# Kernel optimization log

Hardware: AMD Instinct MI355X
Metric: run time of the kernel (lower is better)

The kernel has to match this reference:

```python
import jax, jax.numpy as jnp
import numpy as np

RADIUS = 0.4
NSAMPLE = 32
B, N, NPOINT, C = 4, 16384, 4096, 64


def _ball_query(xyz, new_xyz, radius, nsample):
    """PointNet++ ball query: first `nsample` point indices (in original order)
    within `radius` of each query; pad with the first found index (0 if none).
    xyz: (B,N,3)  new_xyz: (B,M,3)  ->  idx: (B,M,nsample) int32."""
    n = xyz.shape[1]
    # squared distances (B, M, N) via ||a||^2 + ||b||^2 - 2 a.b
    qq = jnp.sum(new_xyz * new_xyz, axis=-1)[:, :, None]
    pp = jnp.sum(xyz * xyz, axis=-1)[:, None, :]
    d2 = qq + pp - 2.0 * jnp.einsum('bmd,bnd->bmn', new_xyz, xyz)
    ar = jnp.arange(n, dtype=jnp.int32)
    # key = point index if inside ball else sentinel n; smallest keys = earliest hits
    key = jnp.where(d2 < radius * radius, ar, n)
    neg_small, _ = jax.lax.top_k(-key, nsample)   # nsample smallest keys
    sel = -neg_small                               # (B, M, nsample)
    valid = sel < n
    first = jnp.where(valid[..., :1], sel[..., :1], 0)
    return jnp.where(valid, sel, first).astype(jnp.int32)


def setup_inputs() -> dict:
    key = jax.random.key(0)
    k1, k2, k3 = jax.random.split(key, 3)
    xyz = jax.random.normal(k1, (B, N, 3), dtype=jnp.float32)
    new_xyz = jax.random.normal(k2, (B, NPOINT, 3), dtype=jnp.float32)
    features = jax.random.normal(k3, (B, C, N), dtype=jnp.float32)
    return {"xyz": xyz, "new_xyz": new_xyz, "features": features}


def reference(xyz, new_xyz, features):
    idx = _ball_query(xyz, new_xyz, RADIUS, NSAMPLE)            # (B, M, S)
    # gather xyz -> (B, M, S, 3) -> (B, 3, M, S), center on queries
    grouped_xyz = jax.vmap(lambda p, i: p[i])(xyz, idx)
    grouped_xyz = jnp.transpose(grouped_xyz, (0, 3, 1, 2))
    grouped_xyz = grouped_xyz - jnp.transpose(new_xyz, (0, 2, 1))[..., None]
    # gather features -> (B, C, M, S)
    grouped_feat = jax.vmap(lambda f, i: f[:, i])(features, idx)
    # use_xyz=True: concat centered coords with features on channel dim
    return jnp.concatenate([grouped_xyz, grouped_feat], axis=1)  # (B, 3+C, M, S)
```

## Files before the change

### kernel.cpp

```cpp
#include <hip/hip_runtime.h>
#include <stdint.h>

#define B_ 4
#define N_ 16384
#define M_ 4096
#define C_ 64
#define S_ 32
#define R2_ 0.16f
#define GDIM 32
#define CELLS 32768
#define CSTRIDE 32772

static const size_t OFF_XYZ4  = 0;
static const size_t OFF_FT    = (size_t)B_ * N_ * 4 * sizeof(float);
static const size_t OFF_IDX   = OFF_FT + (size_t)B_ * N_ * C_ * sizeof(float);
static const size_t OFF_START = OFF_FT;
static const size_t OFF_CUR   = OFF_START + (size_t)B_ * CSTRIDE * sizeof(int);
static const size_t OFF_SPTS  = OFF_CUR + (size_t)B_ * CSTRIDE * sizeof(int);
static const size_t OFF_SSID  = OFF_SPTS + (size_t)B_ * N_ * 4 * sizeof(float);

__device__ __forceinline__ int cellof(float v) {
    int c = (int)floorf((v + 8.0f) * 2.0f);
    return c < 0 ? 0 : (c > GDIM - 1 ? GDIM - 1 : c);
}

__global__ __launch_bounds__(256) void pack_hist(const float* __restrict__ xyz,
                                                 float4* __restrict__ xyz4,
                                                 int* __restrict__ cur) {
    int i = blockIdx.x * 256 + threadIdx.x;
    int b = i >> 14;
    float x = xyz[3 * i + 0];
    float y = xyz[3 * i + 1];
    float z = xyz[3 * i + 2];
    float pp = __fadd_rn(__fadd_rn(__fmul_rn(x, x), __fmul_rn(y, y)), __fmul_rn(z, z));
    xyz4[i] = make_float4(x, y, z, pp);
    int cid = (cellof(z) << 10) | (cellof(y) << 5) | cellof(x);
    atomicAdd(&cur[b * CSTRIDE + cid], 1);
}

__global__ __launch_bounds__(1024) void scan_cells(int* __restrict__ cur,
                                                   int* __restrict__ start) {
    __shared__ int ls[16];
    int b = blockIdx.x, t = threadIdx.x;
    int lane = t & 63, w = t >> 6;
    int* cb = cur + b * CSTRIDE;
    int* sb = start + b * CSTRIDE;
    int base = t * 32;
    int loc[32]; int tot = 0;
    #pragma unroll
    for (int j = 0; j < 32; ++j) { loc[j] = cb[base + j]; tot += loc[j]; }
    int pre = tot;
    #pragma unroll
    for (int o = 1; o < 64; o <<= 1) { int u = __shfl_up(pre, o); if (lane >= o) pre += u; }
    if (lane == 63) ls[w] = pre;
    __syncthreads();
    if (t < 16) {
        int v = ls[t];
        int p16 = v;
        #pragma unroll
        for (int o = 1; o < 16; o <<= 1) { int u = __shfl_up(p16, o); if (t >= o) p16 += u; }
        ls[t] = p16 - v;
    }
    __syncthreads();
    int run = ls[w] + (pre - tot);
    #pragma unroll
    for (int j = 0; j < 32; ++j) { sb[base + j] = run; cb[base + j] = run; run += loc[j]; }
    if (t == 0) sb[CELLS] = N_;
}

__global__ __launch_bounds__(256) void scatter_pts(const float4* __restrict__ xyz4,
                                                   int* __restrict__ cur,
                                                   float4* __restrict__ spts,
                                                   int* __restrict__ ssid) {
    int i = blockIdx.x * 256 + threadIdx.x;
    int b = i >> 14, n = i & (N_ - 1);
    float4 P = xyz4[i];
    int cid = (cellof(P.z) << 10) | (cellof(P.y) << 5) | cellof(P.x);
    int pos = atomicAdd(&cur[b * CSTRIDE + cid], 1);
    spts[(size_t)b * N_ + pos] = P;
    ssid[b * N_ + pos] = n;
}

__global__ __launch_bounds__(256) void ball_query_grid(const float4* __restrict__ spts,
                                                       const int* __restrict__ ssid,
                                                       const int* __restrict__ start,
                                                       const float* __restrict__ newxyz,
                                                       int* __restrict__ idx) {
    __shared__ unsigned int bmAll[4][512];
    __shared__ int bcAll[4];
    int tid = threadIdx.x, lane = tid & 63, w = tid >> 6;
    unsigned int* bm = bmAll[w];
    int gw = blockIdx.x * 4 + w;
    int b = gw >> 12;
    int m = gw & (M_ - 1);

    *(uint4*)&bm[lane * 8]     = make_uint4(0u, 0u, 0u, 0u);
    *(uint4*)&bm[lane * 8 + 4] = make_uint4(0u, 0u, 0u, 0u);
    if (lane == 0) bcAll[w] = 0;

    size_t qb = ((size_t)b * M_ + m) * 3;
    float qx = newxyz[qb + 0], qy = newxyz[qb + 1], qz = newxyz[qb + 2];
    float qq = __fadd_rn(__fadd_rn(__fmul_rn(qx, qx), __fmul_rn(qy, qy)), __fmul_rn(qz, qz));
    int cx = cellof(qx), cy = cellof(qy), cz = cellof(qz);
    const float4* sp  = spts + (size_t)b * N_;
    const int*    sid = ssid + b * N_;
    const int*    st  = start + b * CSTRIDE;
    int x0 = cx > 0 ? cx - 1 : 0;
    int x1 = cx < GDIM - 1 ? cx + 1 : GDIM - 1;

    int sv = 0, ev = 0;
    if (lane < 9) {
        int dzi = lane / 3, dyi = lane - dzi * 3;
        int nz = cz + dzi - 1, ny = cy + dyi - 1;
        if ((unsigned)nz < GDIM && (unsigned)ny < GDIM) {
            int rowb = (nz << 10) | (ny << 5);
            sv = st[rowb | x0];
            ev = st[(rowb | x1) + 1];
        }
    }
    __builtin_amdgcn_wave_barrier();

    #pragma unroll 1
    for (int j = 0; j < 9; ++j) {
        int s = __shfl(sv, j);
        int e = __shfl(ev, j);
        for (int i = s + lane; i < e; i += 64) {
            float4 P = sp[i];
            float dot = __fmaf_rn(qz, P.z, __fmaf_rn(qy, P.y, __fmul_rn(qx, P.x)));
            float d2  = __fsub_rn(__fadd_rn(qq, P.w), __fmul_rn(2.0f, dot));
            if (d2 < R2_) {
                int o = sid[i];
                atomicOr(&bm[o >> 5], 1u << (o & 31));
            }
        }
    }
    __builtin_amdgcn_wave_barrier();

    uint4 a = *(const uint4*)&bm[lane * 8];
    uint4 c = *(const uint4*)&bm[lane * 8 + 4];
    unsigned int wds[8] = {a.x, a.y, a.z, a.w, c.x, c.y, c.z, c.w};
    int tl = 0;
    #pragma unroll
    for (int j = 0; j < 8; ++j) tl += __popc(wds[j]);
    int pre = tl;
    #pragma unroll
    for (int o = 1; o < 64; o <<= 1) { int u = __shfl_up(pre, o); if (lane >= o) pre += u; }
    int cnt = __shfl(pre, 63);
    int r = pre - tl;
    int* outp = idx + ((size_t)b * M_ + m) * S_;
    int basei = lane << 8;
    #pragma unroll
    for (int wd = 0; wd < 8; ++wd) {
        if (r >= S_) break;
        unsigned int bits = wds[wd];
        while (bits && r < S_) {
            int bpos = __builtin_ctz(bits);
            bits &= bits - 1;
            int gidx = basei + (wd << 5) + bpos;
            if (r == 0) bcAll[w] = gidx;
            outp[r] = gidx;
            ++r;
        }
    }
    __builtin_amdgcn_wave_barrier();
    int firstv = bcAll[w];
    if (lane < S_ && lane >= cnt) outp[lane] = firstv;
}

__global__ __launch_bounds__(256) void transpose_feat(const float* __restrict__ f,
                                                      float* __restrict__ ft) {
    __shared__ float tile[64][65];
    int b  = blockIdx.x >> 8;
    int n0 = (blockIdx.x & 255) << 6;
    int tid  = threadIdx.x;
    int lane = tid & 63;
    int grp  = tid >> 6;
    #pragma unroll
    for (int r = 0; r < 16; ++r) {
        int c = r * 4 + grp;
        tile[c][lane] = f[((size_t)b * C_ + c) * N_ + n0 + lane];
    }
    __syncthreads();
    #pragma unroll
    for (int r = 0; r < 16; ++r) {
        int nl = r * 4 + grp;
        ft[((size_t)b * N_ + n0 + nl) * C_ + lane] = tile[lane][nl];
    }
}

__global__ __launch_bounds__(256) void group_out(const float4* __restrict__ xyz4,
                                                 const float* __restrict__ ft,
                                                 const float* __restrict__ newxyz,
                                                 const int* __restrict__ idx,
                                                 float* __restrict__ out) {
    __shared__ int   sidx[32];
    __shared__ float q[3];
    int tid = threadIdx.x;
    int b   = blockIdx.x >> 12;
    int m   = blockIdx.x & 4095;
    if (tid < 32) sidx[tid] = idx[((size_t)b * M_ + m) * S_ + tid];
    if (tid < 3)  q[tid]    = newxyz[((size_t)b * M_ + m) * 3 + tid];
    __syncthreads();

    int s  = tid & 31;
    int c8 = tid >> 5;
    int p  = sidx[s];

    const float* fp = ft + ((size_t)b * N_ + p) * C_ + c8 * 8;
    float4 v0 = *(const float4*)(fp);
    float4 v1 = *(const float4*)(fp + 4);

    const size_t st = (size_t)M_ * S_;
    size_t ob = (((size_t)b * 67 + 3 + c8 * 8) * M_ + m) * S_ + s;
    out[ob + 0 * st] = v0.x;
    out[ob + 1 * st] = v0.y;
    out[ob + 2 * st] = v0.z;
    out[ob + 3 * st] = v0.w;
    out[ob + 4 * st] = v1.x;
    out[ob + 5 * st] = v1.y;
    out[ob + 6 * st] = v1.z;
    out[ob + 7 * st] = v1.w;

    if (tid < 32) {
        float4 P = xyz4[(size_t)b * N_ + p];
        size_t xb = (((size_t)b * 67 + 0) * M_ + m) * S_ + s;
        out[xb + 0 * st] = P.x - q[0];
        out[xb + 1 * st] = P.y - q[1];
        out[xb + 2 * st] = P.z - q[2];
    }
}

extern "C" void kernel_launch(void* const* d_in, const int* in_sizes, int n_in,
                              void* d_out, int out_size, void* d_ws, size_t ws_size,
                              hipStream_t stream) {
    const float* xyz    = (const float*)d_in[0];
    const float* newxyz = (const float*)d_in[1];
    const float* feat   = (const float*)d_in[2];
    float* out = (float*)d_out;

    char* ws = (char*)d_ws;
    float4* xyz4  = (float4*)(ws + OFF_XYZ4);
    float*  ft    = (float*)(ws + OFF_FT);
    int*    idxb  = (int*)(ws + OFF_IDX);
    int*    startc= (int*)(ws + OFF_START);
    int*    curc  = (int*)(ws + OFF_CUR);
    float4* spts  = (float4*)(ws + OFF_SPTS);
    int*    ssid  = (int*)(ws + OFF_SSID);

    hipMemsetAsync(curc, 0, (size_t)B_ * CSTRIDE * sizeof(int), stream);
    pack_hist     <<<(B_ * N_) / 256, 256, 0, stream>>>(xyz, xyz4, curc);
    scan_cells    <<<B_, 1024, 0, stream>>>(curc, startc);
    scatter_pts   <<<(B_ * N_) / 256, 256, 0, stream>>>(xyz4, curc, spts, ssid);
    ball_query_grid<<<(B_ * M_) / 4, 256, 0, stream>>>(spts, ssid, startc, newxyz, idxb);
    transpose_feat<<<B_ * (N_ / 64), 256, 0, stream>>>(feat, ft);
    group_out     <<<B_ * M_, 256, 0, stream>>>(xyz4, ft, newxyz, idxb, out);
}
```

Before: 229.3 us.

## Fuse ball query with grouping output, keep neighbor indices in LDS

```diff
diff --git a/kernel.cpp b/kernel.cpp
--- a/kernel.cpp
+++ b/kernel.cpp
@@ -13,8 +13,7 @@
 
 static const size_t OFF_XYZ4  = 0;
 static const size_t OFF_FT    = (size_t)B_ * N_ * 4 * sizeof(float);
-static const size_t OFF_IDX   = OFF_FT + (size_t)B_ * N_ * C_ * sizeof(float);
-static const size_t OFF_START = OFF_FT;
+static const size_t OFF_START = OFF_FT + (size_t)B_ * N_ * C_ * sizeof(float);
 static const size_t OFF_CUR   = OFF_START + (size_t)B_ * CSTRIDE * sizeof(int);
 static const size_t OFF_SPTS  = OFF_CUR + (size_t)B_ * CSTRIDE * sizeof(int);
 static const size_t OFF_SSID  = OFF_SPTS + (size_t)B_ * N_ * 4 * sizeof(float);
@@ -81,11 +80,34 @@
     ssid[b * N_ + pos] = n;
 }
 
-__global__ __launch_bounds__(256) void ball_query_grid(const float4* __restrict__ spts,
-                                                       const int* __restrict__ ssid,
-                                                       const int* __restrict__ start,
-                                                       const float* __restrict__ newxyz,
-                                                       int* __restrict__ idx) {
+__global__ __launch_bounds__(256) void transpose_feat(const float* __restrict__ f,
+                                                      float* __restrict__ ft) {
+    __shared__ float tile[64][65];
+    int b  = blockIdx.x >> 8;
+    int n0 = (blockIdx.x & 255) << 6;
+    int tid  = threadIdx.x;
+    int lane = tid & 63;
+    int grp  = tid >> 6;
+    #pragma unroll
+    for (int r = 0; r < 16; ++r) {
+        int c = r * 4 + grp;
+        tile[c][lane] = f[((size_t)b * C_ + c) * N_ + n0 + lane];
+    }
+    __syncthreads();
+    #pragma unroll
+    for (int r = 0; r < 16; ++r) {
+        int nl = r * 4 + grp;
+        ft[((size_t)b * N_ + n0 + nl) * C_ + lane] = tile[lane][nl];
+    }
+}
+
+__global__ __launch_bounds__(256) void bq_group(const float4* __restrict__ spts,
+                                                const int* __restrict__ ssid,
+                                                const int* __restrict__ start,
+                                                const float* __restrict__ newxyz,
+                                                const float4* __restrict__ xyz4,
+                                                const float* __restrict__ ft,
+                                                float* __restrict__ out) {
     __shared__ unsigned int bmAll[4][512];
     __shared__ int bcAll[4];
     int tid = threadIdx.x, lane = tid & 63, w = tid >> 6;
@@ -147,8 +169,9 @@
     for (int o = 1; o < 64; o <<= 1) { int u = __shfl_up(pre, o); if (lane >= o) pre += u; }
     int cnt = __shfl(pre, 63);
     int r = pre - tl;
-    int* outp = idx + ((size_t)b * M_ + m) * S_;
     int basei = lane << 8;
+    __builtin_amdgcn_wave_barrier();
+    int* sel = (int*)bm;
     #pragma unroll
     for (int wd = 0; wd < 8; ++wd) {
         if (r >= S_) break;
@@ -158,75 +181,37 @@
             bits &= bits - 1;
             int gidx = basei + (wd << 5) + bpos;
             if (r == 0) bcAll[w] = gidx;
-            outp[r] = gidx;
+            sel[r] = gidx;
             ++r;
         }
     }
     __builtin_amdgcn_wave_barrier();
-    int firstv = bcAll[w];
-    if (lane < S_ && lane >= cnt) outp[lane] = firstv;
-}
-
-__global__ __launch_bounds__(256) void transpose_feat(const float* __restrict__ f,
-                                                      float* __restrict__ ft) {
-    __shared__ float tile[64][65];
-    int b  = blockIdx.x >> 8;
-    int n0 = (blockIdx.x & 255) << 6;
-    int tid  = threadIdx.x;
-    int lane = tid & 63;
-    int grp  = tid >> 6;
-    #pragma unroll
-    for (int r = 0; r < 16; ++r) {
-        int c = r * 4 + grp;
-        tile[c][lane] = f[((size_t)b * C_ + c) * N_ + n0 + lane];
-    }
-    __syncthreads();
-    #pragma unroll
-    for (int r = 0; r < 16; ++r) {
-        int nl = r * 4 + grp;
-        ft[((size_t)b * N_ + n0 + nl) * C_ + lane] = tile[lane][nl];
-    }
-}
-
-__global__ __launch_bounds__(256) void group_out(const float4* __restrict__ xyz4,
-                                                 const float* __restrict__ ft,
-                                                 const float* __restrict__ newxyz,
-                                                 const int* __restrict__ idx,
-                                                 float* __restrict__ out) {
-    __shared__ int   sidx[32];
-    __shared__ float q[3];
-    int tid = threadIdx.x;
-    int b   = blockIdx.x >> 12;
-    int m   = blockIdx.x & 4095;
-    if (tid < 32) sidx[tid] = idx[((size_t)b * M_ + m) * S_ + tid];
-    if (tid < 3)  q[tid]    = newxyz[((size_t)b * M_ + m) * 3 + tid];
-    __syncthreads();
-
-    int s  = tid & 31;
-    int c8 = tid >> 5;
-    int p  = sidx[s];
-
-    const float* fp = ft + ((size_t)b * N_ + p) * C_ + c8 * 8;
-    float4 v0 = *(const float4*)(fp);
-    float4 v1 = *(const float4*)(fp + 4);
-
-    const size_t st = (size_t)M_ * S_;
-    size_t ob = (((size_t)b * 67 + 3 + c8 * 8) * M_ + m) * S_ + s;
-    out[ob + 0 * st] = v0.x;
-    out[ob + 1 * st] = v0.y;
-    out[ob + 2 * st] = v0.z;
-    out[ob + 3 * st] = v0.w;
-    out[ob + 4 * st] = v1.x;
-    out[ob + 5 * st] = v1.y;
-    out[ob + 6 * st] = v1.z;
-    out[ob + 7 * st] = v1.w;
-
-    if (tid < 32) {
+    if (lane < S_ && lane >= cnt) sel[lane] = bcAll[w];
+    __builtin_amdgcn_wave_barrier();
+
+    int s    = lane & 31;
+    int half = lane >> 5;
+    int p    = sel[s];
+    const float* fp = ft + (((size_t)b * N_ + p) << 6) + half * 32;
+    float4 v[8];
+    #pragma unroll
+    for (int j = 0; j < 8; ++j) v[j] = *(const float4*)(fp + j * 4);
+
+    const size_t cst = (size_t)M_ * S_;
+    size_t ob = (((size_t)b * 67 + 3 + half * 32) * M_ + m) * S_ + s;
+    #pragma unroll
+    for (int j = 0; j < 8; ++j) {
+        out[ob + (4 * j + 0) * cst] = v[j].x;
+        out[ob + (4 * j + 1) * cst] = v[j].y;
+        out[ob + (4 * j + 2) * cst] = v[j].z;
+        out[ob + (4 * j + 3) * cst] = v[j].w;
+    }
+    if (half == 0) {
         float4 P = xyz4[(size_t)b * N_ + p];
         size_t xb = (((size_t)b * 67 + 0) * M_ + m) * S_ + s;
-        out[xb + 0 * st] = P.x - q[0];
-        out[xb + 1 * st] = P.y - q[1];
-        out[xb + 2 * st] = P.z - q[2];
+        out[xb + 0 * cst] = P.x - qx;
+        out[xb + 1 * cst] = P.y - qy;
+        out[xb + 2 * cst] = P.z - qz;
     }
 }
 
@@ -241,7 +226,6 @@
     char* ws = (char*)d_ws;
     float4* xyz4  = (float4*)(ws + OFF_XYZ4);
     float*  ft    = (float*)(ws + OFF_FT);
-    int*    idxb  = (int*)(ws + OFF_IDX);
     int*    startc= (int*)(ws + OFF_START);
     int*    curc  = (int*)(ws + OFF_CUR);
     float4* spts  = (float4*)(ws + OFF_SPTS);
@@ -251,7 +235,7 @@
     pack_hist     <<<(B_ * N_) / 256, 256, 0, stream>>>(xyz, xyz4, curc);
     scan_cells    <<<B_, 1024, 0, stream>>>(curc, startc);
     scatter_pts   <<<(B_ * N_) / 256, 256, 0, stream>>>(xyz4, curc, spts, ssid);
-    ball_query_grid<<<(B_ * M_) / 4, 256, 0, stream>>>(spts, ssid, startc, newxyz, idxb);
     transpose_feat<<<B_ * (N_ / 64), 256, 0, stream>>>(feat, ft);
-    group_out     <<<B_ * M_, 256, 0, stream>>>(xyz4, ft, newxyz, idxb, out);
-}
+    bq_group      <<<(B_ * M_) / 4, 256, 0, stream>>>(spts, ssid, startc, newxyz,
+                                                      xyz4, ft, out);
+}
```

New measurement: 220.6 us. -3.8%, faster.
